# Kernel tuning notes

Hardware: AMD Instinct MI355X
Metric: run time of the kernel (lower is better)

Reference implementation:

```python
import jax, jax.numpy as jnp
import numpy as np

N, D, F, M, K = 4096, 1024, 4096, 2048, 307
EPS = 1e-5

def _ln(h, g, b):
    mu = jnp.mean(h, axis=-1, keepdims=True)
    var = jnp.mean(jnp.square(h - mu), axis=-1, keepdims=True)
    return (h - mu) * jax.lax.rsqrt(var + EPS) * g + b

def _attn(h, wq, wk, wv, mask):
    # wq/wk/wv stored as [D, D] so y = h @ w matches torch Linear(h) with W.T
    q = h @ wq
    k = h @ wk
    v = h @ wv
    s = (q @ k.T) * (1.0 / np.sqrt(D))  # [N, N]
    s = jnp.where(mask, -1e9, s)
    a = jax.nn.softmax(s, axis=-1)
    return a @ v, a

def _ffn(h, w1, b1, w2, b2):
    return jax.nn.gelu(h @ w1 + b1, approximate=False) @ w2 + b2

def setup_inputs() -> dict:
    ks = jax.random.split(jax.random.key(0), 32)
    s = 0.02
    p = lambda i, shape: (jax.random.normal(ks[i], shape, jnp.float32) * s)
    inp = {
        'x': jax.random.normal(ks[0], (N, D), jnp.float32),
        'real_edge_mask': jax.random.bernoulli(ks[1], 0.5, (N, N)),
        'fake_edge_mask': jax.random.bernoulli(ks[2], 0.5, (N, N)),
        'mask_nodes': jax.random.permutation(ks[3], N)[:M].astype(jnp.int32),
        'gene_idx': jnp.argsort(jax.random.uniform(ks[4], (M, D)), axis=-1)[:, :K].astype(jnp.int32),
        'wq1': p(5, (D, D)), 'wk1': p(6, (D, D)), 'wv1': p(7, (D, D)),
        'g1': jnp.ones((D,)), 'be1': jnp.zeros((D,)),
        'fw1': p(8, (D, F)), 'fb1': jnp.zeros((F,)),
        'fw2': p(9, (F, D)), 'fb2': jnp.zeros((D,)),
        'g2': jnp.ones((D,)), 'be2': jnp.zeros((D,)),
        'wq2': p(10, (D, D)), 'wk2': p(11, (D, D)), 'wv2': p(12, (D, D)),
        'g3': jnp.ones((D,)), 'be3': jnp.zeros((D,)),
        'hw1': p(13, (D, F)), 'hb1': jnp.zeros((F,)),
        'hw2': p(14, (F, D)), 'hb2': jnp.zeros((D,)),
        'g4': jnp.ones((D,)), 'be4': jnp.zeros((D,)),
        'head_w': p(15, (D, D)), 'head_b': jnp.zeros((D,)),
    }
    return inp

def reference(x, real_edge_mask, fake_edge_mask, mask_nodes, gene_idx,
              wq1, wk1, wv1, g1, be1, fw1, fb1, fw2, fb2, g2, be2,
              wq2, wk2, wv2, g3, be3, hw1, hb1, hw2, hb2, g4, be4,
              head_w, head_b):
    rows = jnp.arange(M)[:, None]  # [M, 1]
    # encoding_mask_nodes: zero K genes in each of M masked cells
    mask_x = x[mask_nodes].at[rows, gene_idx].set(0.0)
    use_x = x.at[mask_nodes].set(mask_x)

    hidden, encode_weights = _attn(use_x, wq1, wk1, wv1, real_edge_mask)
    hidden = _ln(hidden + use_x, g1, be1)
    hidden = _ln(hidden + _ffn(hidden, fw1, fb1, fw2, fb2), g2, be2)
    # NOTE: original `hidden[mask_nodes][gene_mask] = 0` is a no-op (copy), reproduced.

    recon, _decode_weights = _attn(hidden, wq2, wk2, wv2, real_edge_mask)
    recon = _ln(recon + hidden, g3, be3)
    recon = _ln(recon + _ffn(recon, hw1, hb1, hw2, hb2), g4, be4)
    h = recon @ head_w + head_b

    x_init = x[mask_nodes][rows, gene_idx]   # [M, K]
    x_recon = h[mask_nodes][rows, gene_idx]  # [M, K]
    return x_init, x_recon, encode_weights, recon
```

## Files before the change

kernel.cpp:

```cpp
#include <hip/hip_runtime.h>
#include <math.h>
#include <stdint.h>

typedef unsigned short u16;
typedef __attribute__((ext_vector_type(8))) short bf16x8;
typedef __attribute__((ext_vector_type(4))) float f32x4;

#define N_ 4096
#define D_ 1024
#define F_ 4096
#define M_ 2048
#define KG 307

__device__ __forceinline__ u16 f2bf(float f) {
  unsigned int u = __float_as_uint(f);
  unsigned int r = u + 0x7fffu + ((u >> 16) & 1u);
  return (u16)(r >> 16);
}

__device__ __forceinline__ void gl_lds16(const u16* g, u16* l) {
  __builtin_amdgcn_global_load_lds(
      (__attribute__((address_space(1))) void*)(void*)g,
      (__attribute__((address_space(3))) void*)(void*)l,
      16, 0, 0);
}

enum { E_QKV = 0, E_SMASK = 1, E_PART = 2, E_GELU = 3 };

template <int EPI>
__global__ __launch_bounds__(256, 4) void gemm_nt(
    const u16* __restrict__ A, const u16* __restrict__ B,
    void* __restrict__ C, void* __restrict__ C2,
    int Ndim, int Ksp, int lda, int ldb, long zstr,
    const float* __restrict__ bias, const unsigned char* __restrict__ mask,
    float scale) {
  __shared__ u16 As[2][128 * 32];
  __shared__ u16 Bs[2][128 * 32];
  const int tid = threadIdx.x;
  const int lane = tid & 63;
  const int wid = tid >> 6;
  const int wr = wid >> 1;
  const int wc = wid & 1;
  const int lr = lane & 15;
  const int lk = lane >> 4;
  const long bm = (long)blockIdx.x * 128;
  const long bn = (long)blockIdx.y * 128;
  const long koff = (long)blockIdx.z * Ksp;

  f32x4 acc[4][4];
#pragma unroll
  for (int i = 0; i < 4; ++i)
#pragma unroll
    for (int j = 0; j < 4; ++j) acc[i][j] = f32x4{0.f, 0.f, 0.f, 0.f};

  auto stage = [&](int buf, long k0) {
#pragma unroll
    for (int i = 0; i < 2; ++i) {
      int o = tid + i * 256;
      int r = o >> 2, s = o & 3;
      gl_lds16(A + (bm + r) * (long)lda + k0 + ((s ^ ((r >> 1) & 3)) << 3), As[buf] + o * 8);
    }
#pragma unroll
    for (int i = 0; i < 2; ++i) {
      int o = tid + i * 256;
      int r = o >> 2, s = o & 3;
      gl_lds16(B + (bn + r) * (long)ldb + k0 + ((s ^ ((r >> 1) & 3)) << 3), Bs[buf] + o * 8);
    }
  };

  stage(0, koff);
  __syncthreads();
  const int nt = Ksp / 32;
  int cur = 0;
  for (int t = 0; t < nt; ++t) {
    if (t + 1 < nt) stage(cur ^ 1, koff + (long)(t + 1) * 32);
    bf16x8 av[4], bv[4];
#pragma unroll
    for (int mr = 0; mr < 4; ++mr) {
      int r = wr * 64 + mr * 16 + lr;
      av[mr] = *(const bf16x8*)(As[cur] + r * 32 + ((lk ^ ((r >> 1) & 3)) << 3));
    }
#pragma unroll
    for (int nr = 0; nr < 4; ++nr) {
      int r = wc * 64 + nr * 16 + lr;
      bv[nr] = *(const bf16x8*)(Bs[cur] + r * 32 + ((lk ^ ((r >> 1) & 3)) << 3));
    }
#pragma unroll
    for (int mr = 0; mr < 4; ++mr)
#pragma unroll
      for (int nr = 0; nr < 4; ++nr)
        acc[mr][nr] = __builtin_amdgcn_mfma_f32_16x16x32_bf16(av[mr], bv[nr], acc[mr][nr], 0, 0, 0);
    __syncthreads();
    cur ^= 1;
  }

  const bool z0 = (blockIdx.z == 0);
  float* Cz = (float*)C + (long)blockIdx.z * zstr;
#pragma unroll
  for (int mr = 0; mr < 4; ++mr) {
#pragma unroll
    for (int nr = 0; nr < 4; ++nr) {
#pragma unroll
      for (int j = 0; j < 4; ++j) {
        long row = bm + wr * 64 + mr * 16 + lk * 4 + j;
        long col = bn + wc * 64 + nr * 16 + lr;
        float v = acc[mr][nr][j];
        if constexpr (EPI == E_QKV) {
          if (col < 2048)
            ((u16*)C)[row * 2048 + col] = f2bf(v);
          else
            ((u16*)C2)[(col - 2048) * (long)N_ + row] = f2bf(v);
        } else if constexpr (EPI == E_SMASK) {
          v *= scale;
          if (mask[row * Ndim + col]) v = -1e9f;
          ((float*)C)[row * Ndim + col] = v;
        } else if constexpr (EPI == E_PART) {
          Cz[row * Ndim + col] = v + ((z0 && bias) ? bias[col] : 0.f);
        } else if constexpr (EPI == E_GELU) {
          float tv = v + bias[col];
          float gl = 0.5f * tv * (1.0f + erff(tv * 0.70710678118654752f));
          ((u16*)C)[row * Ndim + col] = f2bf(gl);
        }
      }
    }
  }
}

__global__ __launch_bounds__(256) void tcvt(const float* __restrict__ in,
                                            u16* __restrict__ out, int R, int C) {
  __shared__ float tile[32][33];
  int bx = blockIdx.x * 32;
  int by = blockIdx.y * 32;
  int tx = threadIdx.x & 31;
  int ty = threadIdx.x >> 5;
#pragma unroll
  for (int i = 0; i < 32; i += 8)
    tile[ty + i][tx] = in[(long)(by + ty + i) * C + bx + tx];
  __syncthreads();
#pragma unroll
  for (int i = 0; i < 32; i += 8)
    out[(long)(bx + ty + i) * R + by + tx] = f2bf(tile[tx][ty + i]);
}

__global__ void copy_usex(const float* __restrict__ x, float* __restrict__ xf,
                          u16* __restrict__ xb, long n) {
  long i = (long)blockIdx.x * blockDim.x + threadIdx.x;
  if (i < n) {
    float v = x[i];
    xf[i] = v;
    xb[i] = f2bf(v);
  }
}

__global__ void mask_zero(const float* __restrict__ x, const int* __restrict__ mask_nodes,
                          const int* __restrict__ gene_idx, float* __restrict__ xf,
                          u16* __restrict__ xb, float* __restrict__ x_init) {
  int m = blockIdx.x;
  int k = threadIdx.x;
  if (k >= KG) return;
  int row = mask_nodes[m];
  int col = gene_idx[m * KG + k];
  x_init[m * KG + k] = x[(long)row * D_ + col];
  xf[(long)row * D_ + col] = 0.f;
  xb[(long)row * D_ + col] = 0;
}

template <int NY>
__global__ __launch_bounds__(256) void add_ln(const float* __restrict__ y, long ystr,
                                              const float* __restrict__ r,
                                              const float* __restrict__ g,
                                              const float* __restrict__ b,
                                              float* __restrict__ of, u16* __restrict__ ob) {
  int row = blockIdx.x;
  const float* yr = y + (long)row * D_;
  const float* rr = r + (long)row * D_;
  float v[4];
  float s = 0.f, ss = 0.f;
#pragma unroll
  for (int i = 0; i < 4; ++i) {
    int idx = threadIdx.x + i * 256;
    float t = rr[idx];
#pragma unroll
    for (int z = 0; z < NY; ++z) t += yr[z * ystr + idx];
    v[i] = t;
    s += t;
    ss += t * t;
  }
#pragma unroll
  for (int o = 32; o > 0; o >>= 1) {
    s += __shfl_down(s, o, 64);
    ss += __shfl_down(ss, o, 64);
  }
  __shared__ float red[8];
  int wid = threadIdx.x >> 6, lane = threadIdx.x & 63;
  if (lane == 0) {
    red[wid] = s;
    red[4 + wid] = ss;
  }
  __syncthreads();
  if (threadIdx.x == 0) {
    red[0] = red[0] + red[1] + red[2] + red[3];
    red[4] = red[4] + red[5] + red[6] + red[7];
  }
  __syncthreads();
  float mu = red[0] * (1.f / D_);
  float var = red[4] * (1.f / D_) - mu * mu;
  float rs = rsqrtf(var + 1e-5f);
#pragma unroll
  for (int i = 0; i < 4; ++i) {
    int idx = threadIdx.x + i * 256;
    float o = (v[i] - mu) * rs * g[idx] + b[idx];
    of[(long)row * D_ + idx] = o;
    ob[(long)row * D_ + idx] = f2bf(o);
  }
}

template <bool WF32>
__global__ __launch_bounds__(256) void softmax_row(const float* __restrict__ sin,
                                                   float* __restrict__ a32,
                                                   u16* __restrict__ a16) {
  int row = blockIdx.x;
  const float* sr = sin + (long)row * N_;
  float v[16];
  float mx = -3.0e38f;
#pragma unroll
  for (int i = 0; i < 16; ++i) {
    v[i] = sr[threadIdx.x + i * 256];
    mx = fmaxf(mx, v[i]);
  }
#pragma unroll
  for (int o = 32; o > 0; o >>= 1) mx = fmaxf(mx, __shfl_down(mx, o, 64));
  __shared__ float red[8];
  int wid = threadIdx.x >> 6, lane = threadIdx.x & 63;
  if (lane == 0) red[wid] = mx;
  __syncthreads();
  if (threadIdx.x == 0) red[0] = fmaxf(fmaxf(red[0], red[1]), fmaxf(red[2], red[3]));
  __syncthreads();
  mx = red[0];
  float sum = 0.f;
#pragma unroll
  for (int i = 0; i < 16; ++i) {
    v[i] = __expf(v[i] - mx);
    sum += v[i];
  }
#pragma unroll
  for (int o = 32; o > 0; o >>= 1) sum += __shfl_down(sum, o, 64);
  if (lane == 0) red[4 + wid] = sum;
  __syncthreads();
  if (threadIdx.x == 0) red[4] = red[4] + red[5] + red[6] + red[7];
  __syncthreads();
  float inv = 1.f / red[4];
#pragma unroll
  for (int i = 0; i < 16; ++i) {
    float p = v[i] * inv;
    long off = (long)row * N_ + threadIdx.x + i * 256;
    if constexpr (WF32) a32[off] = p;
    a16[off] = f2bf(p);
  }
}

__global__ void gather_rows(const u16* __restrict__ src, const int* __restrict__ mask_nodes,
                            u16* __restrict__ dst) {
  int m = blockIdx.x;
  int row = mask_nodes[m];
  for (int i = threadIdx.x; i < D_; i += 256)
    dst[(long)m * D_ + i] = src[(long)row * D_ + i];
}

__global__ void gather_recon(const float* __restrict__ h, const int* __restrict__ gene_idx,
                             float* __restrict__ xr) {
  int m = blockIdx.x;
  int k = threadIdx.x;
  if (k >= KG) return;
  xr[m * KG + k] = h[(long)m * D_ + gene_idx[m * KG + k]];
}

extern "C" void kernel_launch(void* const* d_in, const int* in_sizes, int n_in,
                              void* d_out, int out_size, void* d_ws, size_t ws_size,
                              hipStream_t stream) {
  const float* x = (const float*)d_in[0];
  const unsigned char* real_mask = (const unsigned char*)d_in[1];
  const int* mask_nodes = (const int*)d_in[3];
  const int* gene_idx = (const int*)d_in[4];
  const float* wq1 = (const float*)d_in[5];
  const float* wk1 = (const float*)d_in[6];
  const float* wv1 = (const float*)d_in[7];
  const float* g1 = (const float*)d_in[8];
  const float* be1 = (const float*)d_in[9];
  const float* fw1 = (const float*)d_in[10];
  const float* fb1 = (const float*)d_in[11];
  const float* fw2 = (const float*)d_in[12];
  const float* fb2 = (const float*)d_in[13];
  const float* g2 = (const float*)d_in[14];
  const float* be2 = (const float*)d_in[15];
  const float* wq2 = (const float*)d_in[16];
  const float* wk2 = (const float*)d_in[17];
  const float* wv2 = (const float*)d_in[18];
  const float* g3 = (const float*)d_in[19];
  const float* be3 = (const float*)d_in[20];
  const float* hw1 = (const float*)d_in[21];
  const float* hb1 = (const float*)d_in[22];
  const float* hw2 = (const float*)d_in[23];
  const float* hb2 = (const float*)d_in[24];
  const float* g4 = (const float*)d_in[25];
  const float* be4 = (const float*)d_in[26];
  const float* head_w = (const float*)d_in[27];
  const float* head_b = (const float*)d_in[28];

  float* out_xinit = (float*)d_out;
  float* out_xrecon = out_xinit + (long)M_ * KG;
  float* out_enc = out_xrecon + (long)M_ * KG;
  float* out_recon = out_enc + (long)N_ * N_;

  char* w = (char*)d_ws;
  size_t off = 0;
  auto alloc = [&](size_t bytes) {
    void* p = w + off;
    off += (bytes + 255) & ~(size_t)255;
    return p;
  };
  float* useXf = (float*)alloc((size_t)N_ * D_ * 4);
  u16* useXb = (u16*)alloc((size_t)N_ * D_ * 2);
  u16* wslot = (u16*)alloc((size_t)D_ * F_ * 2);
  u16* qkb = (u16*)alloc((size_t)N_ * 2048 * 2);
  u16* vT = (u16*)alloc((size_t)D_ * N_ * 2);
  float* sbuf = (float*)alloc((size_t)N_ * N_ * 4);
  u16* aB = (u16*)alloc((size_t)N_ * N_ * 2);
  float* gout4 = (float*)alloc((size_t)4 * N_ * D_ * 4);
  float* actA = (float*)alloc((size_t)N_ * D_ * 4);
  float* actB = (float*)alloc((size_t)N_ * D_ * 4);
  u16* actB16 = (u16*)alloc((size_t)N_ * D_ * 2);
  u16* tbuf = (u16*)sbuf;
  u16* AgB = qkb;

  const float scale = 1.0f / 32.0f;
  const long nd = (long)N_ * D_;
  dim3 blk(256);

  copy_usex<<<dim3((unsigned)((nd + 255) / 256)), blk, 0, stream>>>(x, useXf, useXb, nd);
  mask_zero<<<dim3(M_), 320, 0, stream>>>(x, mask_nodes, gene_idx, useXf, useXb, out_xinit);

#define TCVT(src, R, C, dst) tcvt<<<dim3((C) / 32, (R) / 32), blk, 0, stream>>>(src, dst, R, C)
#define G128(EP, GM, GN, Z, A, B, C, C2, ND, KS, LA, LB, ZS, BI, MK, SC) \
  gemm_nt<EP><<<dim3(GM, GN, Z), blk, 0, stream>>>(A, B, C, C2, ND, KS, LA, LB, ZS, BI, MK, SC)

  TCVT(wq1, D_, D_, wslot);
  TCVT(wk1, D_, D_, wslot + 1024 * 1024);
  TCVT(wv1, D_, D_, wslot + 2048 * 1024);
  G128(E_QKV, 32, 24, 1, useXb, wslot, qkb, vT, 3072, 1024, 1024, 1024, 0, nullptr, nullptr, 0.f);
  G128(E_SMASK, 32, 32, 1, qkb, qkb + 1024, out_enc, nullptr, 4096, 1024, 2048, 2048, 0, nullptr, real_mask, scale);
  softmax_row<true><<<dim3(N_), blk, 0, stream>>>(out_enc, out_enc, aB);
  G128(E_PART, 32, 8, 4, aB, vT, gout4, nullptr, 1024, 1024, 4096, 4096, nd, nullptr, nullptr, 0.f);
  add_ln<4><<<dim3(N_), blk, 0, stream>>>(gout4, nd, useXf, g1, be1, actA, actB16);
  TCVT(fw1, D_, F_, wslot);
  G128(E_GELU, 32, 32, 1, actB16, wslot, tbuf, nullptr, 4096, 1024, 1024, 1024, 0, fb1, nullptr, 0.f);
  TCVT(fw2, F_, D_, wslot);
  G128(E_PART, 32, 8, 4, tbuf, wslot, gout4, nullptr, 1024, 1024, 4096, 4096, nd, fb2, nullptr, 0.f);
  add_ln<4><<<dim3(N_), blk, 0, stream>>>(gout4, nd, actA, g2, be2, actB, actB16);

  TCVT(wq2, D_, D_, wslot);
  TCVT(wk2, D_, D_, wslot + 1024 * 1024);
  TCVT(wv2, D_, D_, wslot + 2048 * 1024);
  G128(E_QKV, 32, 24, 1, actB16, wslot, qkb, vT, 3072, 1024, 1024, 1024, 0, nullptr, nullptr, 0.f);
  G128(E_SMASK, 32, 32, 1, qkb, qkb + 1024, sbuf, nullptr, 4096, 1024, 2048, 2048, 0, nullptr, real_mask, scale);
  softmax_row<false><<<dim3(N_), blk, 0, stream>>>(sbuf, nullptr, aB);
  G128(E_PART, 32, 8, 4, aB, vT, gout4, nullptr, 1024, 1024, 4096, 4096, nd, nullptr, nullptr, 0.f);
  add_ln<4><<<dim3(N_), blk, 0, stream>>>(gout4, nd, actB, g3, be3, actA, actB16);
  TCVT(hw1, D_, F_, wslot);
  G128(E_GELU, 32, 32, 1, actB16, wslot, tbuf, nullptr, 4096, 1024, 1024, 1024, 0, hb1, nullptr, 0.f);
  TCVT(hw2, F_, D_, wslot);
  G128(E_PART, 32, 8, 4, tbuf, wslot, gout4, nullptr, 1024, 1024, 4096, 4096, nd, hb2, nullptr, 0.f);
  add_ln<4><<<dim3(N_), blk, 0, stream>>>(gout4, nd, actA, g4, be4, out_recon, actB16);

  gather_rows<<<dim3(M_), blk, 0, stream>>>(actB16, mask_nodes, AgB);
  TCVT(head_w, D_, D_, wslot);
  G128(E_PART, 16, 8, 1, AgB, wslot, gout4, nullptr, 1024, 1024, 1024, 1024, 0, head_b, nullptr, 0.f);
  gather_recon<<<dim3(M_), 320, 0, stream>>>(gout4, gene_idx, out_xrecon);
#undef TCVT
#undef G128
}
```

Baseline: 708.4 us.

## Triple-buffer GEMM K-loop with explicit vmcnt waits and batch QKV weight conversion

The GEMM mainloop changes from double buffering with __syncthreads to a three-slot LDS ring. Loads are issued three K-tiles ahead, and the code waits on vmcnt counts before a raw s_barrier, so more global-to-LDS traffic is in flight while the MFMAs run. LDS use rises to 48KB per block and the occupancy hint drops from 4 to 3 blocks. Separately, the three Q/K/V weight transposes are merged into one launch using blockIdx.z, which saves two launches per attention layer. The hand-set vmcnt counts assume every stage issues exactly four loads per thread.

```diff
diff --git a/kernel.cpp b/kernel.cpp
--- a/kernel.cpp
+++ b/kernel.cpp
@@ -28,14 +28,14 @@
 enum { E_QKV = 0, E_SMASK = 1, E_PART = 2, E_GELU = 3 };
 
 template <int EPI>
-__global__ __launch_bounds__(256, 4) void gemm_nt(
+__global__ __launch_bounds__(256, 3) void gemm_nt(
     const u16* __restrict__ A, const u16* __restrict__ B,
     void* __restrict__ C, void* __restrict__ C2,
     int Ndim, int Ksp, int lda, int ldb, long zstr,
     const float* __restrict__ bias, const unsigned char* __restrict__ mask,
     float scale) {
-  __shared__ u16 As[2][128 * 32];
-  __shared__ u16 Bs[2][128 * 32];
+  __shared__ u16 As[3][128 * 32];
+  __shared__ u16 Bs[3][128 * 32];
   const int tid = threadIdx.x;
   const int lane = tid & 63;
   const int wid = tid >> 6;
@@ -53,45 +53,60 @@
 #pragma unroll
     for (int j = 0; j < 4; ++j) acc[i][j] = f32x4{0.f, 0.f, 0.f, 0.f};
 
-  auto stage = [&](int buf, long k0) {
+  auto stage = [&](int sl, long k0) {
 #pragma unroll
     for (int i = 0; i < 2; ++i) {
       int o = tid + i * 256;
       int r = o >> 2, s = o & 3;
-      gl_lds16(A + (bm + r) * (long)lda + k0 + ((s ^ ((r >> 1) & 3)) << 3), As[buf] + o * 8);
+      gl_lds16(A + (bm + r) * (long)lda + k0 + ((s ^ ((r >> 1) & 3)) << 3), As[sl] + o * 8);
     }
 #pragma unroll
     for (int i = 0; i < 2; ++i) {
       int o = tid + i * 256;
       int r = o >> 2, s = o & 3;
-      gl_lds16(B + (bn + r) * (long)ldb + k0 + ((s ^ ((r >> 1) & 3)) << 3), Bs[buf] + o * 8);
+      gl_lds16(B + (bn + r) * (long)ldb + k0 + ((s ^ ((r >> 1) & 3)) << 3), Bs[sl] + o * 8);
     }
   };
 
+  const int nt = Ksp / 32;
   stage(0, koff);
-  __syncthreads();
-  const int nt = Ksp / 32;
-  int cur = 0;
+  stage(1, koff + 32);
+  stage(2, koff + 64);
+  __builtin_amdgcn_sched_barrier(0);
+
+  int sl = 0;
   for (int t = 0; t < nt; ++t) {
-    if (t + 1 < nt) stage(cur ^ 1, koff + (long)(t + 1) * 32);
+    const int left = nt - 1 - t;
+    if (left >= 2)
+      asm volatile("s_waitcnt vmcnt(8)");
+    else if (left == 1)
+      asm volatile("s_waitcnt vmcnt(4)");
+    else
+      asm volatile("s_waitcnt vmcnt(0)");
+    __builtin_amdgcn_sched_barrier(0);
+    __builtin_amdgcn_s_barrier();
+
     bf16x8 av[4], bv[4];
 #pragma unroll
     for (int mr = 0; mr < 4; ++mr) {
       int r = wr * 64 + mr * 16 + lr;
-      av[mr] = *(const bf16x8*)(As[cur] + r * 32 + ((lk ^ ((r >> 1) & 3)) << 3));
+      av[mr] = *(const bf16x8*)(As[sl] + r * 32 + ((lk ^ ((r >> 1) & 3)) << 3));
     }
 #pragma unroll
     for (int nr = 0; nr < 4; ++nr) {
       int r = wc * 64 + nr * 16 + lr;
-      bv[nr] = *(const bf16x8*)(Bs[cur] + r * 32 + ((lk ^ ((r >> 1) & 3)) << 3));
+      bv[nr] = *(const bf16x8*)(Bs[sl] + r * 32 + ((lk ^ ((r >> 1) & 3)) << 3));
     }
 #pragma unroll
     for (int mr = 0; mr < 4; ++mr)
 #pragma unroll
       for (int nr = 0; nr < 4; ++nr)
         acc[mr][nr] = __builtin_amdgcn_mfma_f32_16x16x32_bf16(av[mr], bv[nr], acc[mr][nr], 0, 0, 0);
-    __syncthreads();
-    cur ^= 1;
+    __builtin_amdgcn_s_barrier();
+    __builtin_amdgcn_sched_barrier(0);
+    if (t + 3 < nt) stage(sl, koff + (long)(t + 3) * 32);
+    __builtin_amdgcn_sched_barrier(0);
+    sl = (sl == 2) ? 0 : sl + 1;
   }
 
   const bool z0 = (blockIdx.z == 0);
@@ -126,9 +141,13 @@
   }
 }
 
-__global__ __launch_bounds__(256) void tcvt(const float* __restrict__ in,
-                                            u16* __restrict__ out, int R, int C) {
+__global__ __launch_bounds__(256) void tcvt3(const float* __restrict__ in0,
+                                             const float* __restrict__ in1,
+                                             const float* __restrict__ in2,
+                                             u16* __restrict__ out, int R, int C) {
   __shared__ float tile[32][33];
+  const float* in = (blockIdx.z == 0) ? in0 : (blockIdx.z == 1 ? in1 : in2);
+  u16* dst = out + (size_t)blockIdx.z * R * C;
   int bx = blockIdx.x * 32;
   int by = blockIdx.y * 32;
   int tx = threadIdx.x & 31;
@@ -139,7 +158,7 @@
   __syncthreads();
 #pragma unroll
   for (int i = 0; i < 32; i += 8)
-    out[(long)(bx + ty + i) * R + by + tx] = f2bf(tile[tx][ty + i]);
+    dst[(long)(bx + ty + i) * R + by + tx] = f2bf(tile[tx][ty + i]);
 }
 
 __global__ void copy_usex(const float* __restrict__ x, float* __restrict__ xf,
@@ -340,42 +359,42 @@
   copy_usex<<<dim3((unsigned)((nd + 255) / 256)), blk, 0, stream>>>(x, useXf, useXb, nd);
   mask_zero<<<dim3(M_), 320, 0, stream>>>(x, mask_nodes, gene_idx, useXf, useXb, out_xinit);
 
-#define TCVT(src, R, C, dst) tcvt<<<dim3((C) / 32, (R) / 32), blk, 0, stream>>>(src, dst, R, C)
+#define TCVT1(src, R, C, dst) \
+  tcvt3<<<dim3((C) / 32, (R) / 32, 1), blk, 0, stream>>>(src, src, src, dst, R, C)
+#define TCVTQ(s0, s1, s2, dst) \
+  tcvt3<<<dim3(32, 32, 3), blk, 0, stream>>>(s0, s1, s2, dst, 1024, 1024)
 #define G128(EP, GM, GN, Z, A, B, C, C2, ND, KS, LA, LB, ZS, BI, MK, SC) \
   gemm_nt<EP><<<dim3(GM, GN, Z), blk, 0, stream>>>(A, B, C, C2, ND, KS, LA, LB, ZS, BI, MK, SC)
 
-  TCVT(wq1, D_, D_, wslot);
-  TCVT(wk1, D_, D_, wslot + 1024 * 1024);
-  TCVT(wv1, D_, D_, wslot + 2048 * 1024);
+  TCVTQ(wq1, wk1, wv1, wslot);
   G128(E_QKV, 32, 24, 1, useXb, wslot, qkb, vT, 3072, 1024, 1024, 1024, 0, nullptr, nullptr, 0.f);
   G128(E_SMASK, 32, 32, 1, qkb, qkb + 1024, out_enc, nullptr, 4096, 1024, 2048, 2048, 0, nullptr, real_mask, scale);
   softmax_row<true><<<dim3(N_), blk, 0, stream>>>(out_enc, out_enc, aB);
   G128(E_PART, 32, 8, 4, aB, vT, gout4, nullptr, 1024, 1024, 4096, 4096, nd, nullptr, nullptr, 0.f);
   add_ln<4><<<dim3(N_), blk, 0, stream>>>(gout4, nd, useXf, g1, be1, actA, actB16);
-  TCVT(fw1, D_, F_, wslot);
+  TCVT1(fw1, D_, F_, wslot);
   G128(E_GELU, 32, 32, 1, actB16, wslot, tbuf, nullptr, 4096, 1024, 1024, 1024, 0, fb1, nullptr, 0.f);
-  TCVT(fw2, F_, D_, wslot);
+  TCVT1(fw2, F_, D_, wslot);
   G128(E_PART, 32, 8, 4, tbuf, wslot, gout4, nullptr, 1024, 1024, 4096, 4096, nd, fb2, nullptr, 0.f);
   add_ln<4><<<dim3(N_), blk, 0, stream>>>(gout4, nd, actA, g2, be2, actB, actB16);
 
-  TCVT(wq2, D_, D_, wslot);
-  TCVT(wk2, D_, D_, wslot + 1024 * 1024);
-  TCVT(wv2, D_, D_, wslot + 2048 * 1024);
+  TCVTQ(wq2, wk2, wv2, wslot);
   G128(E_QKV, 32, 24, 1, actB16, wslot, qkb, vT, 3072, 1024, 1024, 1024, 0, nullptr, nullptr, 0.f);
   G128(E_SMASK, 32, 32, 1, qkb, qkb + 1024, sbuf, nullptr, 4096, 1024, 2048, 2048, 0, nullptr, real_mask, scale);
   softmax_row<false><<<dim3(N_), blk, 0, stream>>>(sbuf, nullptr, aB);
   G128(E_PART, 32, 8, 4, aB, vT, gout4, nullptr, 1024, 1024, 4096, 4096, nd, nullptr, nullptr, 0.f);
   add_ln<4><<<dim3(N_), blk, 0, stream>>>(gout4, nd, actB, g3, be3, actA, actB16);
-  TCVT(hw1, D_, F_, wslot);
+  TCVT1(hw1, D_, F_, wslot);
   G128(E_GELU, 32, 32, 1, actB16, wslot, tbuf, nullptr, 4096, 1024, 1024, 1024, 0, hb1, nullptr, 0.f);
-  TCVT(hw2, F_, D_, wslot);
+  TCVT1(hw2, F_, D_, wslot);
   G128(E_PART, 32, 8, 4, tbuf, wslot, gout4, nullptr, 1024, 1024, 4096, 4096, nd, hb2, nullptr, 0.f);
   add_ln<4><<<dim3(N_), blk, 0, stream>>>(gout4, nd, actA, g4, be4, out_recon, actB16);
 
   gather_rows<<<dim3(M_), blk, 0, stream>>>(actB16, mask_nodes, AgB);
-  TCVT(head_w, D_, D_, wslot);
+  TCVT1(head_w, D_, D_, wslot);
   G128(E_PART, 16, 8, 1, AgB, wslot, gout4, nullptr, 1024, 1024, 1024, 1024, 0, head_b, nullptr, 0.f);
   gather_recon<<<dim3(M_), 320, 0, stream>>>(gout4, gene_idx, out_xrecon);
-#undef TCVT
+#undef TCVT1
+#undef TCVTQ
 #undef G128
 }
```

Result: slower. 780.6 us (+10.2%).
